# Optimization experiments

Measured on AMD Instinct MI355X. Metric: run time of the kernel, lower is better.

Reference implementation:

```python
import jax, jax.numpy as jnp
import numpy as np

H, DH = 12, 64
D = H * DH
EPS = 1e-5
NEG = -10000.0


def _layernorm(x, gamma, beta):
    mu = jnp.mean(x, axis=-1, keepdims=True)
    var = jnp.mean(jnp.square(x - mu), axis=-1, keepdims=True)
    return (x - mu) * jax.lax.rsqrt(var + EPS) * gamma + beta


def setup_inputs() -> dict:
    key = jax.random.key(0)
    ks = jax.random.split(key, 10)
    B, E, L = 1, 64, 256
    x = jax.random.normal(ks[0], (B, E, L, D), dtype=jnp.float32)
    padding_mask = jax.random.bernoulli(ks[1], 0.1, (B, E, L))
    s = 1.0 / np.sqrt(D)
    w_row = jax.random.normal(ks[2], (3 * D, D), dtype=jnp.float32) * s
    b_row = jnp.zeros((3 * D,), dtype=jnp.float32)
    w_col = jax.random.normal(ks[3], (3 * D, D), dtype=jnp.float32) * s
    b_col = jnp.zeros((3 * D,), dtype=jnp.float32)
    gamma1 = jnp.ones((D,), dtype=jnp.float32)
    beta1 = jnp.zeros((D,), dtype=jnp.float32)
    gamma2 = jnp.ones((D,), dtype=jnp.float32)
    beta2 = jnp.zeros((D,), dtype=jnp.float32)
    return {"x": x, "padding_mask": padding_mask, "w_row": w_row, "b_row": b_row,
            "w_col": w_col, "b_col": b_col, "gamma1": gamma1, "beta1": beta1,
            "gamma2": gamma2, "beta2": beta2}


def _qkv(x, w, b, B, E, L):
    qkv = x @ w.T + b  # [B,E,L,3D]
    q, k, v = jnp.split(qkv, 3, axis=-1)
    rs = lambda t: t.reshape(B, E, L, H, DH)
    return rs(q), rs(k), rs(v)


def reference(x, padding_mask, w_row, b_row, w_col, b_col, gamma1, beta1, gamma2, beta2):
    B, E, L, _ = x.shape
    mask = jnp.where(padding_mask, NEG, 0.0).astype(x.dtype)  # [B,E,L], same per head

    # ---- tied row attention ----
    q, k, v = _qkv(x, w_row, b_row, B, E, L)
    q = q * (DH * E) ** (-0.5)
    row_logits = jnp.einsum('bsihc,bsjhc->bhij', q, k)  # [B,H,L,L], tied over E
    row_logits = row_logits + mask.sum(axis=1)[:, None, None, :]  # sum over E, bcast over i,h
    row_maps = jax.nn.softmax(row_logits, axis=-1)
    row_out = jnp.einsum('bhij,bsjhc->bsihc', row_maps, v).reshape(B, E, L, D)
    out = _layernorm(x + row_out, gamma1, beta1)

    # ---- column attention ----
    q, k, v = _qkv(out, w_col, b_col, B, E, L)
    q = q * DH ** (-0.5)
    col_logits = jnp.einsum('bilhc,bjlhc->bhijl', q, k)  # [B,H,E,E,L]
    col_logits = col_logits + mask[:, None, None, :, :]  # bcast over h,i; applied along j
    col_maps = jax.nn.softmax(col_logits, axis=-2)
    col_out = jnp.einsum('bhijl,bjlhc->bilhc', col_maps, v).reshape(B, E, L, D)
    out = _layernorm(out + col_out, gamma2, beta2)

    return out, row_maps[:, :, None, :, :]  # row maps returned as [B,H,1,L,L]
```

## Files before the change

### kernel.cpp

```cpp
#include <hip/hip_runtime.h>
#include <hip/hip_bf16.h>
#include <float.h>

#define E_  64
#define L_  256
#define D_  768
#define H_  12
#define DH_ 64
#define TD_ 2304
#define NEGV -10000.0f
#define EPS_ 1e-5f

#define GM 16384
#define GN 2304
#define GK 768

#define RSPLIT 8

typedef __attribute__((ext_vector_type(8))) __bf16 bf16x8;
typedef __attribute__((ext_vector_type(4))) float f32x4;
typedef __attribute__((ext_vector_type(8))) unsigned short u16x8;

__device__ __forceinline__ float wred_sum64(float v){
  #pragma unroll
  for (int o = 32; o > 0; o >>= 1) v += __shfl_xor(v, o, 64);
  return v;
}
__device__ __forceinline__ float wred_max64(float v){
  #pragma unroll
  for (int o = 32; o > 0; o >>= 1) v = fmaxf(v, __shfl_xor(v, o, 64));
  return v;
}
__device__ __forceinline__ unsigned short f2bf(float f){
  unsigned int u = __float_as_uint(f);
  u += 0x7FFF + ((u >> 16) & 1);
  return (unsigned short)(u >> 16);
}
__device__ __forceinline__ float bf2f(unsigned short s){
  return __uint_as_float(((unsigned int)s) << 16);
}

__global__ __launch_bounds__(256) void f2b_kernel(
    const float* __restrict__ in, unsigned short* __restrict__ out){
  size_t i = ((size_t)blockIdx.x * 256 + threadIdx.x) * 8;
  float4 a = *(const float4*)(in + i);
  float4 b = *(const float4*)(in + i + 4);
  u16x8 o;
  o[0]=f2bf(a.x); o[1]=f2bf(a.y); o[2]=f2bf(a.z); o[3]=f2bf(a.w);
  o[4]=f2bf(b.x); o[5]=f2bf(b.y); o[6]=f2bf(b.z); o[7]=f2bf(b.w);
  *(u16x8*)(out + i) = o;
}

__global__ void masksum_kernel(const int* __restrict__ pm, float* __restrict__ msum){
  int l = threadIdx.x;
  int cnt = 0;
  #pragma unroll
  for (int s = 0; s < E_; ++s) cnt += (pm[s * L_ + l] != 0);
  msum[l] = NEGV * (float)cnt;
}

__global__ __launch_bounds__(256) void gemm_mfma_nt(
    const unsigned short* __restrict__ A,
    const unsigned short* __restrict__ W,
    const float* __restrict__ bias,
    unsigned short* __restrict__ C){
  __shared__ unsigned short As[128*32] __attribute__((aligned(16)));
  __shared__ unsigned short Bs[128*32] __attribute__((aligned(16)));
  int tid = threadIdx.x;
  int lane = tid & 63, wave = tid >> 6;
  int wr = wave >> 1, wc = wave & 1;
  int m0 = blockIdx.y * 128, n0 = blockIdx.x * 128;
  int col16 = lane & 15, kgrp = lane >> 4;

  f32x4 zero = {0.f, 0.f, 0.f, 0.f};
  f32x4 acc[4][4];
  #pragma unroll
  for (int mf = 0; mf < 4; ++mf)
    #pragma unroll
    for (int nf = 0; nf < 4; ++nf) acc[mf][nf] = zero;

  int srow = lane >> 2;
  int kchunk = (lane & 3) * 8;
  const unsigned short* Ag = A + (size_t)(m0 + wave * 32 + srow) * GK + kchunk;
  const unsigned short* Wg = W + (size_t)(n0 + wave * 32 + srow) * GK + kchunk;
  unsigned short* AsB = &As[(wave * 32) * 32];
  unsigned short* BsB = &Bs[(wave * 32) * 32];

  for (int k0 = 0; k0 < GK; k0 += 32) {
    __syncthreads();
    __builtin_amdgcn_global_load_lds(
      (const __attribute__((address_space(1))) unsigned int*)(Ag + k0),
      (__attribute__((address_space(3))) unsigned int*)(AsB), 16, 0, 0);
    __builtin_amdgcn_global_load_lds(
      (const __attribute__((address_space(1))) unsigned int*)(Ag + 16 * GK + k0),
      (__attribute__((address_space(3))) unsigned int*)(AsB + 16 * 32), 16, 0, 0);
    __builtin_amdgcn_global_load_lds(
      (const __attribute__((address_space(1))) unsigned int*)(Wg + k0),
      (__attribute__((address_space(3))) unsigned int*)(BsB), 16, 0, 0);
    __builtin_amdgcn_global_load_lds(
      (const __attribute__((address_space(1))) unsigned int*)(Wg + 16 * GK + k0),
      (__attribute__((address_space(3))) unsigned int*)(BsB + 16 * 32), 16, 0, 0);
    __syncthreads();
    bf16x8 af[4], bfr[4];
    #pragma unroll
    for (int mf = 0; mf < 4; ++mf)
      af[mf] = *(const bf16x8*)&As[(wr * 64 + mf * 16 + col16) * 32 + kgrp * 8];
    #pragma unroll
    for (int nf = 0; nf < 4; ++nf)
      bfr[nf] = *(const bf16x8*)&Bs[(wc * 64 + nf * 16 + col16) * 32 + kgrp * 8];
    #pragma unroll
    for (int mf = 0; mf < 4; ++mf)
      #pragma unroll
      for (int nf = 0; nf < 4; ++nf)
        acc[mf][nf] = __builtin_amdgcn_mfma_f32_16x16x32_bf16(af[mf], bfr[nf], acc[mf][nf], 0, 0, 0);
  }

  float bv[4];
  #pragma unroll
  for (int nf = 0; nf < 4; ++nf) bv[nf] = bias[n0 + wc * 64 + nf * 16 + col16];
  #pragma unroll
  for (int mf = 0; mf < 4; ++mf){
    int rbase = m0 + wr * 64 + mf * 16 + kgrp * 4;
    #pragma unroll
    for (int j = 0; j < 4; ++j){
      unsigned short* crow = C + (size_t)(rbase + j) * GN + n0 + wc * 64 + col16;
      #pragma unroll
      for (int nf = 0; nf < 4; ++nf)
        crow[nf * 16] = f2bf(acc[mf][nf][j] + bv[nf]);
    }
  }
}

__global__ __launch_bounds__(256) void row_logits_mfma(
    const unsigned short* __restrict__ qkvb, float* __restrict__ rlogp){
  __shared__ unsigned short As[128*64] __attribute__((aligned(16)));
  __shared__ unsigned short Bs[128*64] __attribute__((aligned(16)));
  int p = blockIdx.x;
  int tile = blockIdx.y;
  int h = blockIdx.z;
  int i0 = (tile >> 1) * 128, j0 = (tile & 1) * 128;
  int tid = threadIdx.x;
  int lane = tid & 63, wave = tid >> 6;
  int wr = wave >> 1, wc = wave & 1;
  int lanelow = lane & 15, kgrp = lane >> 4;

  f32x4 zero = {0.f, 0.f, 0.f, 0.f};
  f32x4 acc[4][4];
  #pragma unroll
  for (int mf = 0; mf < 4; ++mf)
    #pragma unroll
    for (int nf = 0; nf < 4; ++nf) acc[mf][nf] = zero;

  int cb8 = tid & 7;
  const unsigned short* qb = qkvb + h * DH_;
  const unsigned short* kb = qkvb + D_ + h * DH_;

  for (int ss = 0; ss < E_ / RSPLIT; ++ss){
    int s = p * (E_ / RSPLIT) + ss;
    size_t sb = (size_t)s * L_ * TD_;
    __syncthreads();
    #pragma unroll
    for (int q = 0; q < 4; ++q){
      int row = q * 32 + (tid >> 3);
      int srcoff = (cb8 * 8) ^ ((row & 7) * 8);
      unsigned short* ldsA = &As[(q * 256 + wave * 64) * 8];
      unsigned short* ldsB = &Bs[(q * 256 + wave * 64) * 8];
      __builtin_amdgcn_global_load_lds(
        (const __attribute__((address_space(1))) unsigned int*)(qb + sb + (size_t)(i0 + row) * TD_ + srcoff),
        (__attribute__((address_space(3))) unsigned int*)ldsA, 16, 0, 0);
      __builtin_amdgcn_global_load_lds(
        (const __attribute__((address_space(1))) unsigned int*)(kb + sb + (size_t)(j0 + row) * TD_ + srcoff),
        (__attribute__((address_space(3))) unsigned int*)ldsB, 16, 0, 0);
    }
    __syncthreads();
    #pragma unroll
    for (int c0 = 0; c0 < 64; c0 += 32){
      bf16x8 af[4], bfr[4];
      #pragma unroll
      for (int mf = 0; mf < 4; ++mf){
        int row = wr * 64 + mf * 16 + lanelow;
        af[mf] = *(const bf16x8*)&As[row * 64 + ((c0 + kgrp * 8) ^ ((row & 7) * 8))];
      }
      #pragma unroll
      for (int nf = 0; nf < 4; ++nf){
        int row = wc * 64 + nf * 16 + lanelow;
        bfr[nf] = *(const bf16x8*)&Bs[row * 64 + ((c0 + kgrp * 8) ^ ((row & 7) * 8))];
      }
      #pragma unroll
      for (int mf = 0; mf < 4; ++mf)
        #pragma unroll
        for (int nf = 0; nf < 4; ++nf)
          acc[mf][nf] = __builtin_amdgcn_mfma_f32_16x16x32_bf16(af[mf], bfr[nf], acc[mf][nf], 0, 0, 0);
    }
  }

  float* outp = rlogp + ((size_t)p * H_ + h) * (L_ * L_);
  #pragma unroll
  for (int mf = 0; mf < 4; ++mf){
    int ibase = i0 + wr * 64 + mf * 16 + kgrp * 4;
    #pragma unroll
    for (int j2 = 0; j2 < 4; ++j2){
      float* orow = outp + (size_t)(ibase + j2) * L_ + j0 + wc * 64 + lanelow;
      #pragma unroll
      for (int nf = 0; nf < 4; ++nf)
        orow[nf * 16] = acc[mf][nf][j2];
    }
  }
}

__global__ __launch_bounds__(256) void row_softmax_kernel(
    const float* __restrict__ rlogp, const float* __restrict__ msum,
    float* __restrict__ maps, unsigned short* __restrict__ mapsb){
  int row = blockIdx.x;
  int t = threadIdx.x;
  float v = 0.f;
  #pragma unroll
  for (int pp = 0; pp < RSPLIT; ++pp)
    v += rlogp[(size_t)pp * (H_ * L_ * L_) + (size_t)row * L_ + t];
  v = v * (1.0f / 64.0f) + msum[t];
  __shared__ float red[8];
  float m = wred_max64(v);
  int wid = t >> 6;
  if ((t & 63) == 0) red[wid] = m;
  __syncthreads();
  float bm = fmaxf(fmaxf(red[0], red[1]), fmaxf(red[2], red[3]));
  float e = __expf(v - bm);
  float s = wred_sum64(e);
  if ((t & 63) == 0) red[4 + wid] = s;
  __syncthreads();
  float bs = (red[4] + red[5]) + (red[6] + red[7]);
  float p = e / bs;
  maps[(size_t)row * L_ + t] = p;
  mapsb[(size_t)row * L_ + t] = f2bf(p);
}

__global__ __launch_bounds__(256) void vtrans_kernel(
    const unsigned short* __restrict__ qkvb, unsigned short* __restrict__ vt){
  __shared__ unsigned short T[64 * 265];
  int s = blockIdx.x, h = blockIdx.y;
  int t = threadIdx.x;
  const unsigned short* vb = qkvb + 2 * D_ + h * DH_;
  int jr = t >> 3, c0 = (t & 7) * 8;
  #pragma unroll
  for (int pass = 0; pass < 8; ++pass){
    int j = pass * 32 + jr;
    u16x8 r = *(const u16x8*)(vb + ((size_t)s * L_ + j) * TD_ + c0);
    #pragma unroll
    for (int e = 0; e < 8; ++e) T[(c0 + e) * 265 + j] = r[e];
  }
  __syncthreads();
  unsigned short* ob = vt + ((size_t)(s * H_ + h) * DH_) * L_;
  int c = t >> 2;
  #pragma unroll
  for (int u = 0; u < 8; ++u){
    int j0 = ((t & 3) + u * 4) * 8;
    u16x8 w;
    #pragma unroll
    for (int e = 0; e < 8; ++e) w[e] = T[c * 265 + j0 + e];
    *(u16x8*)(ob + (size_t)c * L_ + j0) = w;
  }
}

__global__ __launch_bounds__(256) void row_pv_mfma(
    const unsigned short* __restrict__ mapsb, const unsigned short* __restrict__ vt,
    const float* __restrict__ x, float* __restrict__ rowtmp){
  __shared__ unsigned short As[256*32] __attribute__((aligned(16)));
  __shared__ unsigned short Bs[64*32] __attribute__((aligned(16)));
  int s = blockIdx.x, h = blockIdx.y;
  int tid = threadIdx.x;
  int lane = tid & 63, wave = tid >> 6;
  int lanelow = lane & 15, kgrp = lane >> 4;

  f32x4 zero = {0.f, 0.f, 0.f, 0.f};
  f32x4 acc[4][4];
  #pragma unroll
  for (int mf = 0; mf < 4; ++mf)
    #pragma unroll
    for (int nf = 0; nf < 4; ++nf) acc[mf][nf] = zero;

  int srow = lane >> 2;
  int kchunk = (lane & 3) * 8;
  const unsigned short* Ag = mapsb + (size_t)h * (L_ * L_) + (size_t)(wave * 64 + srow) * L_ + kchunk;
  const unsigned short* Bg = vt + (((size_t)s * H_ + h) * DH_ + wave * 16 + srow) * L_ + kchunk;
  unsigned short* AsB = &As[(wave * 64) * 32];
  unsigned short* BsB = &Bs[(wave * 16) * 32];

  for (int k0 = 0; k0 < L_; k0 += 32){
    __syncthreads();
    #pragma unroll
    for (int u = 0; u < 4; ++u)
      __builtin_amdgcn_global_load_lds(
        (const __attribute__((address_space(1))) unsigned int*)(Ag + (size_t)u * 16 * L_ + k0),
        (__attribute__((address_space(3))) unsigned int*)(AsB + u * 16 * 32), 16, 0, 0);
    __builtin_amdgcn_global_load_lds(
      (const __attribute__((address_space(1))) unsigned int*)(Bg + k0),
      (__attribute__((address_space(3))) unsigned int*)(BsB), 16, 0, 0);
    __syncthreads();
    bf16x8 af[4], bfr[4];
    #pragma unroll
    for (int mf = 0; mf < 4; ++mf)
      af[mf] = *(const bf16x8*)&As[(wave * 64 + mf * 16 + lanelow) * 32 + kgrp * 8];
    #pragma unroll
    for (int nf = 0; nf < 4; ++nf)
      bfr[nf] = *(const bf16x8*)&Bs[(nf * 16 + lanelow) * 32 + kgrp * 8];
    #pragma unroll
    for (int mf = 0; mf < 4; ++mf)
      #pragma unroll
      for (int nf = 0; nf < 4; ++nf)
        acc[mf][nf] = __builtin_amdgcn_mfma_f32_16x16x32_bf16(af[mf], bfr[nf], acc[mf][nf], 0, 0, 0);
  }

  #pragma unroll
  for (int mf = 0; mf < 4; ++mf){
    int ibase = wave * 64 + mf * 16 + kgrp * 4;
    #pragma unroll
    for (int j2 = 0; j2 < 4; ++j2){
      size_t rb = ((size_t)s * L_ + ibase + j2) * D_ + h * DH_ + lanelow;
      #pragma unroll
      for (int nf = 0; nf < 4; ++nf)
        rowtmp[rb + nf * 16] = acc[mf][nf][j2] + x[rb + nf * 16];
    }
  }
}

__global__ __launch_bounds__(256) void ln1_kernel(
    const float* __restrict__ a,
    const float* __restrict__ g, const float* __restrict__ be,
    unsigned short* __restrict__ outb){
  int row = blockIdx.x;
  int t = threadIdx.x;
  const float* pa = a + (size_t)row * D_;
  float v[3];
  float s1 = 0.f, s2 = 0.f;
  #pragma unroll
  for (int u = 0; u < 3; ++u){
    int c = t + u * 256;
    float xv = pa[c];
    v[u] = xv; s1 += xv; s2 += xv * xv;
  }
  s1 = wred_sum64(s1); s2 = wred_sum64(s2);
  __shared__ float red[8];
  int wid = t >> 6;
  if ((t & 63) == 0){ red[wid] = s1; red[4 + wid] = s2; }
  __syncthreads();
  float ts1 = (red[0] + red[1]) + (red[2] + red[3]);
  float ts2 = (red[4] + red[5]) + (red[6] + red[7]);
  float mu = ts1 * (1.0f / D_);
  float var = ts2 * (1.0f / D_) - mu * mu;
  float rs = rsqrtf(var + EPS_);
  #pragma unroll
  for (int u = 0; u < 3; ++u){
    int c = t + u * 256;
    outb[(size_t)row * D_ + c] = f2bf((v[u] - mu) * rs * g[c] + be[c]);
  }
}

__global__ __launch_bounds__(256) void ln2_kernel(
    const unsigned short* __restrict__ ab,
    const float* __restrict__ b,
    const float* __restrict__ g, const float* __restrict__ be,
    float* __restrict__ out){
  int row = blockIdx.x;
  int t = threadIdx.x;
  const unsigned short* pa = ab + (size_t)row * D_;
  const float* pb = b + (size_t)row * D_;
  float v[3];
  float s1 = 0.f, s2 = 0.f;
  #pragma unroll
  for (int u = 0; u < 3; ++u){
    int c = t + u * 256;
    float xv = bf2f(pa[c]) + pb[c];
    v[u] = xv; s1 += xv; s2 += xv * xv;
  }
  s1 = wred_sum64(s1); s2 = wred_sum64(s2);
  __shared__ float red[8];
  int wid = t >> 6;
  if ((t & 63) == 0){ red[wid] = s1; red[4 + wid] = s2; }
  __syncthreads();
  float ts1 = (red[0] + red[1]) + (red[2] + red[3]);
  float ts2 = (red[4] + red[5]) + (red[6] + red[7]);
  float mu = ts1 * (1.0f / D_);
  float var = ts2 * (1.0f / D_) - mu * mu;
  float rs = rsqrtf(var + EPS_);
  #pragma unroll
  for (int u = 0; u < 3; ++u){
    int c = t + u * 256;
    out[(size_t)row * D_ + c] = (v[u] - mu) * rs * g[c] + be[c];
  }
}

__global__ __launch_bounds__(256) void col_attn_mfma(
    const unsigned short* __restrict__ qkvb, const int* __restrict__ pm,
    float* __restrict__ colout){
  __shared__ unsigned short Qs[64*64] __attribute__((aligned(16)));
  __shared__ unsigned short Ks[64*64] __attribute__((aligned(16)));
  __shared__ unsigned short Vt[64*64] __attribute__((aligned(16)));
  __shared__ unsigned short Ps[64*64] __attribute__((aligned(16)));
  __shared__ float cmask[64];
  int l = blockIdx.x, h = blockIdx.y;
  int tid = threadIdx.x;
  int lane = tid & 63, wave = tid >> 6;
  int lanelow = lane & 15, kgrp = lane >> 4;

  const unsigned short* qb = qkvb + h * DH_;
  const unsigned short* kb = qkvb + D_ + h * DH_;
  const unsigned short* vb = qkvb + 2 * D_ + h * DH_;

  if (tid < 64) cmask[tid] = (pm[tid * L_ + l] != 0) ? NEGV : 0.f;

  {
    int row = tid >> 3, ch = tid & 7;
    #pragma unroll
    for (int pass = 0; pass < 2; ++pass){
      int r2 = row + pass * 32;
      size_t gbase = ((size_t)r2 * L_ + l) * TD_ + ch * 8;
      u16x8 q8 = *(const u16x8*)(qb + gbase);
      u16x8 k8 = *(const u16x8*)(kb + gbase);
      int dst = r2 * 64 + ((ch ^ (r2 & 7)) * 8);
      *(u16x8*)&Qs[dst] = q8;
      *(u16x8*)&Ks[dst] = k8;
    }
  }
  {
    int jr = tid & 31, ch = tid >> 5;
    #pragma unroll
    for (int pass = 0; pass < 2; ++pass){
      int j = jr + pass * 32;
      u16x8 v8 = *(const u16x8*)(vb + ((size_t)j * L_ + l) * TD_ + ch * 8);
      #pragma unroll
      for (int e = 0; e < 8; ++e){
        int c = ch * 8 + e;
        Vt[c * 64 + (((j >> 3) ^ (c & 7)) * 8) + (j & 7)] = v8[e];
      }
    }
  }
  __syncthreads();

  f32x4 zero = {0.f, 0.f, 0.f, 0.f};
  f32x4 acc[4] = {zero, zero, zero, zero};
  int irow = wave * 16 + lanelow;
  #pragma unroll
  for (int ks = 0; ks < 2; ++ks){
    bf16x8 af = *(const bf16x8*)&Qs[irow * 64 + (((ks * 4 + kgrp) ^ (irow & 7)) * 8)];
    #pragma unroll
    for (int nf = 0; nf < 4; ++nf){
      int jrow = nf * 16 + lanelow;
      bf16x8 bk = *(const bf16x8*)&Ks[jrow * 64 + (((ks * 4 + kgrp) ^ (jrow & 7)) * 8)];
      acc[nf] = __builtin_amdgcn_mfma_f32_16x16x32_bf16(af, bk, acc[nf], 0, 0, 0);
    }
  }
  float cm[4];
  #pragma unroll
  for (int nf = 0; nf < 4; ++nf) cm[nf] = cmask[nf * 16 + lanelow];
  #pragma unroll
  for (int r = 0; r < 4; ++r){
    float pvv[4];
    float m = -FLT_MAX;
    #pragma unroll
    for (int nf = 0; nf < 4; ++nf){
      pvv[nf] = acc[nf][r] * 0.125f + cm[nf];
      m = fmaxf(m, pvv[nf]);
    }
    m = fmaxf(m, __shfl_xor(m, 1, 64));
    m = fmaxf(m, __shfl_xor(m, 2, 64));
    m = fmaxf(m, __shfl_xor(m, 4, 64));
    m = fmaxf(m, __shfl_xor(m, 8, 64));
    float s = 0.f;
    #pragma unroll
    for (int nf = 0; nf < 4; ++nf){ pvv[nf] = __expf(pvv[nf] - m); s += pvv[nf]; }
    s += __shfl_xor(s, 1, 64);
    s += __shfl_xor(s, 2, 64);
    s += __shfl_xor(s, 4, 64);
    s += __shfl_xor(s, 8, 64);
    float inv = 1.0f / s;
    int i = wave * 16 + kgrp * 4 + r;
    #pragma unroll
    for (int nf = 0; nf < 4; ++nf){
      int j = nf * 16 + lanelow;
      Ps[i * 64 + (((j >> 3) ^ (i & 7)) * 8) + (j & 7)] = f2bf(pvv[nf] * inv);
    }
  }
  __syncthreads();

  f32x4 acc2[4] = {zero, zero, zero, zero};
  #pragma unroll
  for (int ks = 0; ks < 2; ++ks){
    bf16x8 pa = *(const bf16x8*)&Ps[irow * 64 + (((ks * 4 + kgrp) ^ (irow & 7)) * 8)];
    #pragma unroll
    for (int nf = 0; nf < 4; ++nf){
      int crow = nf * 16 + lanelow;
      bf16x8 bv = *(const bf16x8*)&Vt[crow * 64 + (((ks * 4 + kgrp) ^ (crow & 7)) * 8)];
      acc2[nf] = __builtin_amdgcn_mfma_f32_16x16x32_bf16(pa, bv, acc2[nf], 0, 0, 0);
    }
  }
  #pragma unroll
  for (int r = 0; r < 4; ++r){
    int i = wave * 16 + kgrp * 4 + r;
    size_t ob = ((size_t)i * L_ + l) * D_ + h * DH_ + lanelow;
    #pragma unroll
    for (int nf = 0; nf < 4; ++nf)
      colout[ob + nf * 16] = acc2[nf][r];
  }
}

extern "C" void kernel_launch(void* const* d_in, const int* in_sizes, int n_in,
                              void* d_out, int out_size, void* d_ws, size_t ws_size,
                              hipStream_t stream){
  (void)in_sizes; (void)n_in; (void)out_size; (void)ws_size;
  const float* x     = (const float*)d_in[0];
  const int*   pm    = (const int*)  d_in[1];
  const float* w_row = (const float*)d_in[2];
  const float* b_row = (const float*)d_in[3];
  const float* w_col = (const float*)d_in[4];
  const float* b_col = (const float*)d_in[5];
  const float* g1    = (const float*)d_in[6];
  const float* be1   = (const float*)d_in[7];
  const float* g2    = (const float*)d_in[8];
  const float* be2   = (const float*)d_in[9];

  float* out  = (float*)d_out;
  float* maps = out + (size_t)E_ * L_ * D_;

  float* F    = (float*)d_ws;
  unsigned short* qkvb = (unsigned short*)F;
  float* tmpb = F + 18874368;
  unsigned short* out1b = (unsigned short*)(F + 31457280);
  float* msum = F + 37748736;
  float* rlogp = F + 37748992;
  unsigned short* wrb = (unsigned short*)(F + 44040448);
  unsigned short* wcb = (unsigned short*)(F + 44925184);
  unsigned short* mapsb = (unsigned short*)(F + 45809920);
  unsigned short* vtb = (unsigned short*)(F + 46203136);
  unsigned short* xb  = (unsigned short*)tmpb;

  const int M = E_ * L_;
  const int NX = M * D_;
  const int NW = TD_ * D_;

  masksum_kernel<<<1, 256, 0, stream>>>(pm, msum);
  f2b_kernel<<<NX / 2048, 256, 0, stream>>>(x, xb);
  f2b_kernel<<<NW / 2048, 256, 0, stream>>>(w_row, wrb);
  f2b_kernel<<<NW / 2048, 256, 0, stream>>>(w_col, wcb);

  gemm_mfma_nt<<<dim3(GN/128, GM/128), 256, 0, stream>>>(xb, wrb, b_row, qkvb);
  vtrans_kernel<<<dim3(E_, H_), 256, 0, stream>>>(qkvb, vtb);
  row_logits_mfma<<<dim3(RSPLIT, 4, H_), 256, 0, stream>>>(qkvb, rlogp);
  row_softmax_kernel<<<H_ * L_, 256, 0, stream>>>(rlogp, msum, maps, mapsb);
  row_pv_mfma<<<dim3(E_, H_), 256, 0, stream>>>(mapsb, vtb, x, tmpb);
  ln1_kernel<<<M, 256, 0, stream>>>(tmpb, g1, be1, out1b);
  gemm_mfma_nt<<<dim3(GN/128, GM/128), 256, 0, stream>>>(out1b, wcb, b_col, qkvb);
  col_attn_mfma<<<dim3(L_, H_), 256, 0, stream>>>(qkvb, pm, tmpb);
  ln2_kernel<<<M, 256, 0, stream>>>(out1b, tmpb, g2, be2, out);
}
```

Baseline: 303.1 us.

## Pipeline QKV GEMM with 4-stage LDS ring buffer and swizzled layout

Replaces the single-buffered QKV projection GEMM with a 4-deep LDS ring buffer. Tiles are prefetched three k-steps ahead via direct global-to-LDS loads, with vmcnt waits and one barrier per step instead of two. It also XOR-swizzles the 16-byte k-chunks to reduce LDS bank conflicts on the fragment reads, and raises wave priority around the MFMA block. LDS use grows fourfold, which may cut occupancy, and the hand-counted vmcnt values must match the issued loads exactly.

After: 350.1 us. 1.16x slower.

```diff
diff --git a/kernel.cpp b/kernel.cpp
--- a/kernel.cpp
+++ b/kernel.cpp
@@ -16,6 +16,9 @@
 #define GK 768
 
 #define RSPLIT 8
+#define BKP 32
+#define NTILES (GK / BKP)
+#define BUFSZ 4096
 
 typedef __attribute__((ext_vector_type(8))) __bf16 bf16x8;
 typedef __attribute__((ext_vector_type(4))) float f32x4;
@@ -59,18 +62,18 @@
   msum[l] = NEGV * (float)cnt;
 }
 
-__global__ __launch_bounds__(256) void gemm_mfma_nt(
+__global__ __launch_bounds__(256) void gemm_mfma_pipe(
     const unsigned short* __restrict__ A,
     const unsigned short* __restrict__ W,
     const float* __restrict__ bias,
     unsigned short* __restrict__ C){
-  __shared__ unsigned short As[128*32] __attribute__((aligned(16)));
-  __shared__ unsigned short Bs[128*32] __attribute__((aligned(16)));
+  __shared__ unsigned short As[4 * BUFSZ] __attribute__((aligned(16)));
+  __shared__ unsigned short Bs[4 * BUFSZ] __attribute__((aligned(16)));
   int tid = threadIdx.x;
   int lane = tid & 63, wave = tid >> 6;
   int wr = wave >> 1, wc = wave & 1;
   int m0 = blockIdx.y * 128, n0 = blockIdx.x * 128;
-  int col16 = lane & 15, kgrp = lane >> 4;
+  int lanelow = lane & 15, kgrp = lane >> 4;
 
   f32x4 zero = {0.f, 0.f, 0.f, 0.f};
   f32x4 acc[4][4];
@@ -79,51 +82,82 @@
     #pragma unroll
     for (int nf = 0; nf < 4; ++nf) acc[mf][nf] = zero;
 
-  int srow = lane >> 2;
-  int kchunk = (lane & 3) * 8;
-  const unsigned short* Ag = A + (size_t)(m0 + wave * 32 + srow) * GK + kchunk;
-  const unsigned short* Wg = W + (size_t)(n0 + wave * 32 + srow) * GK + kchunk;
-  unsigned short* AsB = &As[(wave * 32) * 32];
-  unsigned short* BsB = &Bs[(wave * 32) * 32];
-
-  for (int k0 = 0; k0 < GK; k0 += 32) {
-    __syncthreads();
-    __builtin_amdgcn_global_load_lds(
-      (const __attribute__((address_space(1))) unsigned int*)(Ag + k0),
-      (__attribute__((address_space(3))) unsigned int*)(AsB), 16, 0, 0);
-    __builtin_amdgcn_global_load_lds(
-      (const __attribute__((address_space(1))) unsigned int*)(Ag + 16 * GK + k0),
-      (__attribute__((address_space(3))) unsigned int*)(AsB + 16 * 32), 16, 0, 0);
-    __builtin_amdgcn_global_load_lds(
-      (const __attribute__((address_space(1))) unsigned int*)(Wg + k0),
-      (__attribute__((address_space(3))) unsigned int*)(BsB), 16, 0, 0);
-    __builtin_amdgcn_global_load_lds(
-      (const __attribute__((address_space(1))) unsigned int*)(Wg + 16 * GK + k0),
-      (__attribute__((address_space(3))) unsigned int*)(BsB + 16 * 32), 16, 0, 0);
-    __syncthreads();
+  int r_lo = lane >> 2;
+  int sc8 = ((lane & 3) ^ (r_lo & 3)) * 8;
+  const unsigned short* Ag = A + (size_t)(m0 + wave * 32 + r_lo) * GK + sc8;
+  const unsigned short* Wg = W + (size_t)(n0 + wave * 32 + r_lo) * GK + sc8;
+  unsigned short* AsW = &As[wave * 1024];
+  unsigned short* BsW = &Bs[wave * 1024];
+
+#define STAGE_T(t_) { \
+    int b_ = (t_) & 3; int k0_ = (t_) * BKP; \
+    __builtin_amdgcn_global_load_lds( \
+      (const __attribute__((address_space(1))) unsigned int*)(Ag + k0_), \
+      (__attribute__((address_space(3))) unsigned int*)(AsW + b_ * BUFSZ), 16, 0, 0); \
+    __builtin_amdgcn_global_load_lds( \
+      (const __attribute__((address_space(1))) unsigned int*)(Ag + 16 * GK + k0_), \
+      (__attribute__((address_space(3))) unsigned int*)(AsW + b_ * BUFSZ + 512), 16, 0, 0); \
+    __builtin_amdgcn_global_load_lds( \
+      (const __attribute__((address_space(1))) unsigned int*)(Wg + k0_), \
+      (__attribute__((address_space(3))) unsigned int*)(BsW + b_ * BUFSZ), 16, 0, 0); \
+    __builtin_amdgcn_global_load_lds( \
+      (const __attribute__((address_space(1))) unsigned int*)(Wg + 16 * GK + k0_), \
+      (__attribute__((address_space(3))) unsigned int*)(BsW + b_ * BUFSZ + 512), 16, 0, 0); \
+  }
+
+  int swk = (kgrp ^ (lanelow & 3)) * 8;
+  int aoff[4], boff[4];
+  #pragma unroll
+  for (int f = 0; f < 4; ++f){
+    aoff[f] = (wr * 64 + f * 16 + lanelow) * 32 + swk;
+    boff[f] = (wc * 64 + f * 16 + lanelow) * 32 + swk;
+  }
+
+  STAGE_T(0); STAGE_T(1); STAGE_T(2);
+  asm volatile("s_waitcnt vmcnt(8)" ::: "memory");
+  __builtin_amdgcn_s_barrier();
+  __builtin_amdgcn_sched_barrier(0);
+
+  #pragma unroll 1
+  for (int t = 0; t < NTILES; ++t){
+    if (t + 3 < NTILES) STAGE_T(t + 3);
+    const unsigned short* Ab = &As[(t & 3) * BUFSZ];
+    const unsigned short* Bb = &Bs[(t & 3) * BUFSZ];
     bf16x8 af[4], bfr[4];
     #pragma unroll
-    for (int mf = 0; mf < 4; ++mf)
-      af[mf] = *(const bf16x8*)&As[(wr * 64 + mf * 16 + col16) * 32 + kgrp * 8];
-    #pragma unroll
-    for (int nf = 0; nf < 4; ++nf)
-      bfr[nf] = *(const bf16x8*)&Bs[(wc * 64 + nf * 16 + col16) * 32 + kgrp * 8];
+    for (int f = 0; f < 4; ++f){
+      af[f]  = *(const bf16x8*)&Ab[aoff[f]];
+      bfr[f] = *(const bf16x8*)&Bb[boff[f]];
+    }
+    asm volatile("s_waitcnt lgkmcnt(0)" ::: "memory");
+    __builtin_amdgcn_sched_barrier(0);
+    __builtin_amdgcn_s_setprio(1);
     #pragma unroll
     for (int mf = 0; mf < 4; ++mf)
       #pragma unroll
       for (int nf = 0; nf < 4; ++nf)
         acc[mf][nf] = __builtin_amdgcn_mfma_f32_16x16x32_bf16(af[mf], bfr[nf], acc[mf][nf], 0, 0, 0);
-  }
+    __builtin_amdgcn_s_setprio(0);
+    __builtin_amdgcn_sched_barrier(0);
+    if (t < NTILES - 1){
+      if (t <= NTILES - 4)      asm volatile("s_waitcnt vmcnt(8)" ::: "memory");
+      else if (t == NTILES - 3) asm volatile("s_waitcnt vmcnt(4)" ::: "memory");
+      else                      asm volatile("s_waitcnt vmcnt(0)" ::: "memory");
+      __builtin_amdgcn_s_barrier();
+      __builtin_amdgcn_sched_barrier(0);
+    }
+  }
+#undef STAGE_T
 
   float bv[4];
   #pragma unroll
-  for (int nf = 0; nf < 4; ++nf) bv[nf] = bias[n0 + wc * 64 + nf * 16 + col16];
+  for (int nf = 0; nf < 4; ++nf) bv[nf] = bias[n0 + wc * 64 + nf * 16 + lanelow];
   #pragma unroll
   for (int mf = 0; mf < 4; ++mf){
     int rbase = m0 + wr * 64 + mf * 16 + kgrp * 4;
     #pragma unroll
     for (int j = 0; j < 4; ++j){
-      unsigned short* crow = C + (size_t)(rbase + j) * GN + n0 + wc * 64 + col16;
+      unsigned short* crow = C + (size_t)(rbase + j) * GN + n0 + wc * 64 + lanelow;
       #pragma unroll
       for (int nf = 0; nf < 4; ++nf)
         crow[nf * 16] = f2bf(acc[mf][nf][j] + bv[nf]);
@@ -542,13 +576,13 @@
   f2b_kernel<<<NW / 2048, 256, 0, stream>>>(w_row, wrb);
   f2b_kernel<<<NW / 2048, 256, 0, stream>>>(w_col, wcb);
 
-  gemm_mfma_nt<<<dim3(GN/128, GM/128), 256, 0, stream>>>(xb, wrb, b_row, qkvb);
+  gemm_mfma_pipe<<<dim3(GN/128, GM/128), 256, 0, stream>>>(xb, wrb, b_row, qkvb);
   vtrans_kernel<<<dim3(E_, H_), 256, 0, stream>>>(qkvb, vtb);
   row_logits_mfma<<<dim3(RSPLIT, 4, H_), 256, 0, stream>>>(qkvb, rlogp);
   row_softmax_kernel<<<H_ * L_, 256, 0, stream>>>(rlogp, msum, maps, mapsb);
   row_pv_mfma<<<dim3(E_, H_), 256, 0, stream>>>(mapsb, vtb, x, tmpb);
   ln1_kernel<<<M, 256, 0, stream>>>(tmpb, g1, be1, out1b);
-  gemm_mfma_nt<<<dim3(GN/128, GM/128), 256, 0, stream>>>(out1b, wcb, b_col, qkvb);
+  gemm_mfma_pipe<<<dim3(GN/128, GM/128), 256, 0, stream>>>(out1b, wcb, b_col, qkvb);
   col_attn_mfma<<<dim3(L_, H_), 256, 0, stream>>>(qkvb, pm, tmpb);
   ln2_kernel<<<M, 256, 0, stream>>>(out1b, tmpb, g2, be2, out);
 }
```
